# Kernel optimization log

Hardware: AMD Instinct MI355X
Metric: run time of the kernel (lower is better)

## Reference

```python
import jax, jax.numpy as jnp
import numpy as np

B, C, H, W = 32, 512, 32, 32  # in_dims = token_dim = 512, num_heads = 1
D = 512  # token_dim * num_heads
EPS = 1e-12  # torch F.normalize eps


def l2norm(x, axis):
    n = jnp.sqrt(jnp.sum(x * x, axis=axis, keepdims=True))
    return x / jnp.maximum(n, EPS)


def setup_inputs() -> dict:
    key = jax.random.key(0)
    ks = jax.random.split(key, 10)
    s = 1.0 / np.sqrt(D)
    return {
        "x_4d": jax.random.normal(ks[0], (B, C, H, W), dtype=jnp.float32),
        "Wq": jax.random.uniform(ks[1], (D, D), jnp.float32, -s, s),
        "bq": jax.random.uniform(ks[2], (D,), jnp.float32, -s, s),
        "Wk": jax.random.uniform(ks[3], (D, D), jnp.float32, -s, s),
        "bk": jax.random.uniform(ks[4], (D,), jnp.float32, -s, s),
        "w_g": jax.random.normal(ks[5], (D, 1), dtype=jnp.float32),
        "Wp": jax.random.uniform(ks[6], (D, D), jnp.float32, -s, s),
        "bp": jax.random.uniform(ks[7], (D,), jnp.float32, -s, s),
        "Wf": jax.random.uniform(ks[8], (D, D), jnp.float32, -s, s),
        "bf": jax.random.uniform(ks[9], (D,), jnp.float32, -s, s),
    }


def reference(x_4d, Wq, bq, Wk, bk, w_g, Wp, bp, Wf, bf):
    b, c, h, w = x_4d.shape
    n = h * w
    scale = D ** (-0.5)
    x = x_4d.reshape(b, c, n).transpose(0, 2, 1)  # [b, n, c]
    query = l2norm(jnp.einsum("bnc,dc->bnd", x, Wq) + bq, axis=-1)  # [b, n, d]
    key = l2norm(jnp.einsum("bnc,dc->bnd", x, Wk) + bk, axis=-1)    # [b, n, d]
    query_weight = query @ w_g                      # [b, n, 1]
    a = l2norm(query_weight * scale, axis=1)        # normalize over sequence dim
    g = jnp.sum(a * query, axis=1)                  # [b, d] global context
    out = jnp.einsum("bnd,ed->bne", g[:, None, :] * key, Wp) + bp + query
    out = jnp.einsum("bnd,ed->bne", out, Wf) + bf
    return out.transpose(0, 2, 1).reshape(b, c, h, w)
```

## Files before the change

### kernel.cpp

```cpp
#include <hip/hip_runtime.h>
#include <math.h>

#define B_ 32
#define D_ 512
#define N_ 1024
#define T_ 32768
#define SCALE 0.04419417382415922f

typedef unsigned short u16;
typedef __attribute__((ext_vector_type(8))) short bf16x8;
typedef __attribute__((ext_vector_type(4))) float f32x4;
typedef __attribute__((ext_vector_type(8))) unsigned short u16x8;

__device__ __forceinline__ u16 bf16_rn(float f) {
    unsigned u = __float_as_uint(f);
    u += 0x7FFFu + ((u >> 16) & 1u);
    return (u16)(u >> 16);
}
__device__ __forceinline__ float bf16f(u16 h) {
    return __uint_as_float(((unsigned)h) << 16);
}

__device__ __forceinline__ void g2l16(const u16* g, u16* lds) {
    __builtin_amdgcn_global_load_lds(
        (const __attribute__((address_space(1))) unsigned int*)g,
        (__attribute__((address_space(3))) unsigned int*)lds, 16, 0, 0);
}

__device__ __forceinline__ float waveRedSum(float v) {
#pragma unroll
    for (int off = 32; off > 0; off >>= 1) v += __shfl_xor(v, off, 64);
    return v;
}


__global__ __launch_bounds__(256) void convx_k(const float* __restrict__ x,
                                               u16* __restrict__ X) {
    __shared__ float tile[64][65];
    const int tid = threadIdx.x;
    const int n0 = blockIdx.x * 64, c0 = blockIdx.y * 64, b = blockIdx.z;
    const int nl = tid & 63, cl0 = (tid >> 6) * 16;
#pragma unroll
    for (int j = 0; j < 16; ++j)
        tile[cl0 + j][nl] = x[((size_t)(b * D_ + c0 + cl0 + j) << 10) + n0 + nl];
    __syncthreads();
    const int nr = tid >> 2, cb = (tid & 3) * 16;
    const size_t row = (size_t)(b * N_ + n0 + nr) * D_ + c0 + cb;
    u16 th[16];
#pragma unroll
    for (int j = 0; j < 16; ++j) th[j] = bf16_rn(tile[cb + j][nr]);
    *(u16x8*)&X[row]     = *(const u16x8*)&th[0];
    *(u16x8*)&X[row + 8] = *(const u16x8*)&th[8];
}

__global__ __launch_bounds__(256) void convw_k(const float* __restrict__ W0,
                                               const float* __restrict__ W1,
                                               const float* __restrict__ W2,
                                               u16* O0, u16* O1, u16* O2) {
    const int s = blockIdx.y;
    const float* src = (s == 0) ? W0 : ((s == 1) ? W1 : W2);
    u16* O = (s == 0) ? O0 : ((s == 1) ? O1 : O2);
    const size_t i0 = (size_t)blockIdx.x * 2048 + threadIdx.x * 8;
    u16 o[8];
#pragma unroll
    for (int j = 0; j < 8; ++j) o[j] = bf16_rn(src[i0 + j]);
    *(u16x8*)&O[i0] = *(const u16x8*)&o[0];
}


__global__ __launch_bounds__(256) void finalize_k(float* __restrict__ ssqQ,
                                                  float* __restrict__ ssqK,
                                                  float* __restrict__ qwr,
                                                  float* __restrict__ Sb) {
    __shared__ float red[4];
    const int i = blockIdx.x * 256 + threadIdx.x;
    const float rq = 1.f / fmaxf(sqrtf(ssqQ[i]), 1e-12f);
    ssqQ[i] = rq;
    const float rk = 1.f / fmaxf(sqrtf(ssqK[i]), 1e-12f);
    ssqK[i] = rk;
    const float qwp = qwr[i] * rq;
    qwr[i] = qwp * rq;
    float s = qwp * qwp;
    s = waveRedSum(s);
    if ((threadIdx.x & 63) == 0) red[threadIdx.x >> 6] = s;
    __syncthreads();
    if (threadIdx.x == 0)
        atomicAdd(Sb + (blockIdx.x >> 2), red[0] + red[1] + red[2] + red[3]);
}

__global__ __launch_bounds__(512) void gctx_k(const float* __restrict__ qw,
                                              const u16* __restrict__ Qn,
                                              float* __restrict__ g) {
    const int b = blockIdx.y;
    const int n0 = blockIdx.x * 128;
    const int d = threadIdx.x;
    const u16* qp = Qn + ((size_t)b * N_ + n0) * D_ + d;
    const float* wp = qw + (size_t)b * N_ + n0;
    float acc = 0.f;
    for (int n = 0; n < 128; ++n) acc += wp[n] * bf16f(qp[(size_t)n * D_]);
    atomicAdd(g + b * D_ + d, acc);
}

__global__ __launch_bounds__(256) void scalewp_k(const float* __restrict__ Wp,
                                                 const float* __restrict__ g,
                                                 const float* __restrict__ Sb,
                                                 u16* __restrict__ WpG) {
    const int b = blockIdx.y;
    const float fb = SCALE / fmaxf(SCALE * sqrtf(Sb[b]), 1e-12f);
    const size_t f0 = (size_t)blockIdx.x * 2048 + threadIdx.x * 8;
    const int c = (int)(f0 & 511);
    u16 o[8];
#pragma unroll
    for (int j = 0; j < 8; ++j)
        o[j] = bf16_rn(Wp[f0 + j] * g[b * D_ + c + j] * fb);
    *(u16x8*)&WpG[(size_t)b * 262144 + f0] = *(const u16x8*)&o[0];
}

__global__ __launch_bounds__(512) void mgemm0(
        const u16* __restrict__ A, const u16* __restrict__ B0,
        const u16* __restrict__ B1,
        const float* __restrict__ bias0, const float* __restrict__ bias1,
        const float* __restrict__ wg,
        float* __restrict__ ssqQ, float* __restrict__ ssqK,
        float* __restrict__ qwr, u16* uout0, u16* uout1) {
    __shared__ u16 As[128 * 64];
    __shared__ u16 Bs[256 * 64];
    const int tid = threadIdx.x;
    const int l = tid & 63, w = tid >> 6;
    const int gid = blockIdx.x;
    const int xcd = gid & 7;
    const int bx = (gid >> 3) & 3;
    const int by = (gid >> 5) * 8 + xcd;
    const int t0 = by * 128;
    const bool sel = bx >= 2;
    const int e0 = (bx & 1) * 256;
    const u16* B = sel ? B1 : B0;
    const float* bias = sel ? bias1 : bias0;
    u16* uout = sel ? uout1 : uout0;
    float* ssq = sel ? ssqK : ssqQ;

    size_t gA[2], gB[4];
    u16 *ldsA[2], *ldsB[4];
#pragma unroll
    for (int i = 0; i < 2; ++i) {
        const int rr = w * 16 + i * 8 + (l >> 3);
        gA[i] = (size_t)(t0 + rr) * 512 + (((l & 7) ^ (rr & 7)) * 8);
        ldsA[i] = As + (w * 16 + i * 8) * 64;
    }
#pragma unroll
    for (int i = 0; i < 4; ++i) {
        const int rr = w * 32 + i * 8 + (l >> 3);
        gB[i] = (size_t)(e0 + rr) * 512 + (((l & 7) ^ (rr & 7)) * 8);
        ldsB[i] = Bs + (w * 32 + i * 8) * 64;
    }

    const int wr = w >> 2, wc = w & 3, kg = l >> 4, r16 = l & 15;
    int aoff[4][2], boff[4][2];
#pragma unroll
    for (int f = 0; f < 4; ++f)
#pragma unroll
        for (int h = 0; h < 2; ++h) {
            const int ra = wr * 64 + f * 16 + r16;
            aoff[f][h] = ra * 64 + (((h * 4 + kg) ^ (ra & 7)) * 8);
            const int rb = wc * 64 + f * 16 + r16;
            boff[f][h] = rb * 64 + (((h * 4 + kg) ^ (rb & 7)) * 8);
        }

    f32x4 acc[4][4];
#pragma unroll
    for (int i = 0; i < 4; ++i)
#pragma unroll
        for (int j = 0; j < 4; ++j) acc[i][j] = 0.f;

#pragma unroll 1
    for (int c0 = 0; c0 < 512; c0 += 64) {
        __syncthreads();
#pragma unroll
        for (int i = 0; i < 2; ++i) g2l16(A + gA[i] + c0, ldsA[i]);
#pragma unroll
        for (int i = 0; i < 4; ++i) g2l16(B + gB[i] + c0, ldsB[i]);
        __syncthreads();
#pragma unroll
        for (int h = 0; h < 2; ++h) {
            bf16x8 av[4], bv[4];
#pragma unroll
            for (int f = 0; f < 4; ++f) {
                av[f] = *(const bf16x8*)&As[aoff[f][h]];
                bv[f] = *(const bf16x8*)&Bs[boff[f][h]];
            }
#pragma unroll
            for (int i = 0; i < 4; ++i)
#pragma unroll
                for (int j = 0; j < 4; ++j)
                    acc[i][j] = __builtin_amdgcn_mfma_f32_16x16x32_bf16(
                        av[i], bv[j], acc[i][j], 0, 0, 0);
        }
    }

    const int mb = wr * 64 + kg * 4;
    const int nb = wc * 64 + r16;
    float bb[4], wgv[4];
#pragma unroll
    for (int fn = 0; fn < 4; ++fn) {
        const int n = e0 + nb + fn * 16;
        bb[fn] = bias[n];
        wgv[fn] = sel ? 0.f : wg[n];
    }
#pragma unroll
    for (int fm = 0; fm < 4; ++fm) {
#pragma unroll
        for (int q = 0; q < 4; ++q) {
            const int m = t0 + mb + fm * 16 + q;
            float s2 = 0.f, wd = 0.f;
#pragma unroll
            for (int fn = 0; fn < 4; ++fn) {
                const float val = acc[fm][fn][q] + bb[fn];
                uout[(size_t)m * 512 + e0 + nb + fn * 16] = bf16_rn(val);
                s2 += val * val;
                wd += val * wgv[fn];
            }
#pragma unroll
            for (int off = 1; off < 16; off <<= 1) {
                s2 += __shfl_xor(s2, off, 64);
                wd += __shfl_xor(wd, off, 64);
            }
            if (r16 == 0) {
                atomicAdd(ssq + m, s2);
                if (!sel) atomicAdd(qwr + m, wd);
            }
        }
    }
}

template <int MODE>
__global__ __launch_bounds__(256) void mgemm12(
        const u16* __restrict__ A, const u16* __restrict__ B0,
        const float* __restrict__ bias,
        const float* __restrict__ rsA, const float* __restrict__ rsQ,
        u16* uout, float* __restrict__ fout) {
    __shared__ u16 As[128 * 64];
    __shared__ u16 Bs[128 * 64];
    const int tid = threadIdx.x;
    const int l = tid & 63, w = tid >> 6;
    const int gid = blockIdx.x;
    const int xcd = gid & 7;
    const int col = (gid >> 3) & 3;
    const int rowt = (gid >> 5) * 8 + xcd;

    const int t0 = rowt * 128 * (MODE == 1 ? 1 : 2) / (MODE == 1 ? 1 : 2);
    const int tt0 = rowt * 128;
    const int e0 = col * 128;
    const int batch = rowt >> 3;
    const u16* B = (MODE == 1) ? B0 + (size_t)batch * 262144 : B0;
    const int arow0 = (MODE == 2) ? e0 : tt0;
    const int brow0 = (MODE == 2) ? tt0 : e0;

    size_t gA[4], gB[4];
    u16 *ldsA[4], *ldsB[4];
#pragma unroll
    for (int i = 0; i < 4; ++i) {
        const int rr = w * 32 + i * 8 + (l >> 3);
        const int sw = ((l & 7) ^ (rr & 7)) * 8;
        gA[i] = (size_t)(arow0 + rr) * 512 + sw;
        gB[i] = (size_t)(brow0 + rr) * 512 + sw;
        ldsA[i] = As + (w * 32 + i * 8) * 64;
        ldsB[i] = Bs + (w * 32 + i * 8) * 64;
    }

    const int wr = w >> 1, wc = w & 1, kg = l >> 4, r16 = l & 15;
    int aoff[4][2], boff[4][2];
#pragma unroll
    for (int f = 0; f < 4; ++f)
#pragma unroll
        for (int h = 0; h < 2; ++h) {
            const int ra = wr * 64 + f * 16 + r16;
            aoff[f][h] = ra * 64 + (((h * 4 + kg) ^ (ra & 7)) * 8);
            const int rb = wc * 64 + f * 16 + r16;
            boff[f][h] = rb * 64 + (((h * 4 + kg) ^ (rb & 7)) * 8);
        }

    f32x4 acc[4][4];
#pragma unroll
    for (int i = 0; i < 4; ++i)
#pragma unroll
        for (int j = 0; j < 4; ++j) acc[i][j] = 0.f;

#pragma unroll 1
    for (int c0 = 0; c0 < 512; c0 += 64) {
        __syncthreads();
#pragma unroll
        for (int i = 0; i < 4; ++i) {
            g2l16(A + gA[i] + c0, ldsA[i]);
            g2l16(B + gB[i] + c0, ldsB[i]);
        }
        __syncthreads();
#pragma unroll
        for (int h = 0; h < 2; ++h) {
            bf16x8 av[4], bv[4];
#pragma unroll
            for (int f = 0; f < 4; ++f) {
                av[f] = *(const bf16x8*)&As[aoff[f][h]];
                bv[f] = *(const bf16x8*)&Bs[boff[f][h]];
            }
#pragma unroll
            for (int i = 0; i < 4; ++i)
#pragma unroll
                for (int j = 0; j < 4; ++j)
                    acc[i][j] = __builtin_amdgcn_mfma_f32_16x16x32_bf16(
                        av[i], bv[j], acc[i][j], 0, 0, 0);
        }
    }

    const int mb = wr * 64 + kg * 4;
    const int nb = wc * 64 + r16;
    if (MODE == 1) {
#pragma unroll
        for (int fm = 0; fm < 4; ++fm) {
            const int m0 = tt0 + mb + fm * 16;
            const float4 ra4 = *(const float4*)(rsA + m0);
            const float4 rq4 = *(const float4*)(rsQ + m0);
            const float ra_[4] = {ra4.x, ra4.y, ra4.z, ra4.w};
            const float rq_[4] = {rq4.x, rq4.y, rq4.z, rq4.w};
#pragma unroll
            for (int fn = 0; fn < 4; ++fn) {
                const int n = e0 + nb + fn * 16;
                const float bb = bias[n];
#pragma unroll
                for (int q = 0; q < 4; ++q) {
                    const size_t idx = (size_t)(m0 + q) * 512 + n;
                    const float val = acc[fm][fn][q] * ra_[q] + bb +
                                      bf16f(uout[idx]) * rq_[q];
                    uout[idx] = bf16_rn(val);
                }
            }
        }
    } else {
#pragma unroll
        for (int fm = 0; fm < 4; ++fm)
#pragma unroll
            for (int fn = 0; fn < 4; ++fn) {
                const int ntok = (tt0 & 1023) + nb + fn * 16;
#pragma unroll
                for (int q = 0; q < 4; ++q) {
                    const int e = e0 + mb + fm * 16 + q;
                    fout[((size_t)(batch * D_ + e) << 10) + ntok] =
                        acc[fm][fn][q] + bias[e];
                }
            }
    }
}


extern "C" void kernel_launch(void* const* d_in, const int* in_sizes, int n_in,
                              void* d_out, int out_size, void* d_ws, size_t ws_size,
                              hipStream_t stream) {
    const float* x  = (const float*)d_in[0];
    const float* Wq = (const float*)d_in[1];
    const float* bq = (const float*)d_in[2];
    const float* Wk = (const float*)d_in[3];
    const float* bk = (const float*)d_in[4];
    const float* wg = (const float*)d_in[5];
    const float* Wp = (const float*)d_in[6];
    const float* bp = (const float*)d_in[7];
    const float* Wf = (const float*)d_in[8];
    const float* bf = (const float*)d_in[9];
    float* out = (float*)d_out;

    char* Wb = (char*)d_ws;
    u16* Xbf = (u16*)Wb;
    u16* WpG = (u16*)Wb;
    u16* Qn  = (u16*)(Wb + 33554432ull);
    u16* Kn  = (u16*)(Wb + 67108864ull);
    char* S  = Wb + 100663296ull;
    u16* Wqbf = (u16*)S;
    u16* Wkbf = (u16*)(S + 524288ull);
    u16* Wfbf = (u16*)(S + 1048576ull);
    char* Z   = S + 1572864ull;
    float* SSQQ = (float*)Z;
    float* SSQK = (float*)(Z + 131072ull);
    float* QWR  = (float*)(Z + 262144ull);
    float* G    = (float*)(Z + 393216ull);
    float* Sb   = (float*)(Z + 458752ull);
    const size_t ZBYTES = 458752ull + 128ull;

    const dim3 blk(256);

    convx_k<<<dim3(16, 8, 32), blk, 0, stream>>>(x, Xbf);
    convw_k<<<dim3(128, 3), blk, 0, stream>>>(Wq, Wk, Wf, Wqbf, Wkbf, Wfbf);
    hipMemsetAsync(Z, 0, ZBYTES, stream);
    mgemm0<<<dim3(1024), dim3(512), 0, stream>>>(Xbf, Wqbf, Wkbf, bq, bk, wg,
                                                 SSQQ, SSQK, QWR, Qn, Kn);
    finalize_k<<<dim3(128), blk, 0, stream>>>(SSQQ, SSQK, QWR, Sb);
    gctx_k<<<dim3(8, B_), dim3(512), 0, stream>>>(QWR, Qn, G);
    scalewp_k<<<dim3(128, B_), blk, 0, stream>>>(Wp, G, Sb, WpG);
    mgemm12<1><<<dim3(1024), blk, 0, stream>>>(Kn, WpG, bp, SSQK, SSQQ, Qn,
                                               nullptr);
    mgemm12<2><<<dim3(1024), blk, 0, stream>>>(Wfbf, Qn, bf, nullptr, nullptr,
                                               nullptr, out);
}
```

Baseline: 157.1 us.

## Fuse x transpose and bf16 conversion into QK GEMM; remap MODE1 grid by batch

Removes the standalone convx_k kernel. The QK GEMM now reads fp32 x directly in its native [b,c,n] layout, converts it to bf16 in registers and writes it transposed into a padded LDS tile. The next K-slice of x is prefetched into registers while the current tile is consumed, and launch bounds request more waves. Separately, the MODE 1 GEMM block mapping groups the tiles of each batch on the same XCD, aiming at better cache reuse of the per-batch scaled Wp. In exchange, the conversion work is repeated across column blocks and x loads are strided, so global read traffic in the GEMM rises.

```diff
diff --git a/kernel.cpp b/kernel.cpp
--- a/kernel.cpp
+++ b/kernel.cpp
@@ -33,25 +33,6 @@
     return v;
 }
 
-
-__global__ __launch_bounds__(256) void convx_k(const float* __restrict__ x,
-                                               u16* __restrict__ X) {
-    __shared__ float tile[64][65];
-    const int tid = threadIdx.x;
-    const int n0 = blockIdx.x * 64, c0 = blockIdx.y * 64, b = blockIdx.z;
-    const int nl = tid & 63, cl0 = (tid >> 6) * 16;
-#pragma unroll
-    for (int j = 0; j < 16; ++j)
-        tile[cl0 + j][nl] = x[((size_t)(b * D_ + c0 + cl0 + j) << 10) + n0 + nl];
-    __syncthreads();
-    const int nr = tid >> 2, cb = (tid & 3) * 16;
-    const size_t row = (size_t)(b * N_ + n0 + nr) * D_ + c0 + cb;
-    u16 th[16];
-#pragma unroll
-    for (int j = 0; j < 16; ++j) th[j] = bf16_rn(tile[cb + j][nr]);
-    *(u16x8*)&X[row]     = *(const u16x8*)&th[0];
-    *(u16x8*)&X[row + 8] = *(const u16x8*)&th[8];
-}
 
 __global__ __launch_bounds__(256) void convw_k(const float* __restrict__ W0,
                                                const float* __restrict__ W1,
@@ -116,14 +97,14 @@
     *(u16x8*)&WpG[(size_t)b * 262144 + f0] = *(const u16x8*)&o[0];
 }
 
-__global__ __launch_bounds__(512) void mgemm0(
-        const u16* __restrict__ A, const u16* __restrict__ B0,
+__global__ __launch_bounds__(512, 4) void mgemm0(
+        const float* __restrict__ x, const u16* __restrict__ B0,
         const u16* __restrict__ B1,
         const float* __restrict__ bias0, const float* __restrict__ bias1,
         const float* __restrict__ wg,
         float* __restrict__ ssqQ, float* __restrict__ ssqK,
         float* __restrict__ qwr, u16* uout0, u16* uout1) {
-    __shared__ u16 As[128 * 64];
+    __shared__ u16 As[128 * 72];
     __shared__ u16 Bs[256 * 64];
     const int tid = threadIdx.x;
     const int l = tid & 63, w = tid >> 6;
@@ -139,14 +120,12 @@
     u16* uout = sel ? uout1 : uout0;
     float* ssq = sel ? ssqK : ssqQ;
 
-    size_t gA[2], gB[4];
-    u16 *ldsA[2], *ldsB[4];
-#pragma unroll
-    for (int i = 0; i < 2; ++i) {
-        const int rr = w * 16 + i * 8 + (l >> 3);
-        gA[i] = (size_t)(t0 + rr) * 512 + (((l & 7) ^ (rr & 7)) * 8);
-        ldsA[i] = As + (w * 16 + i * 8) * 64;
-    }
+    const int tr = tid & 127;
+    const int csl = (tid >> 7) * 16;
+    const float* xrow = x + (((size_t)((t0 >> 10) * D_ + csl)) << 10) +
+                        (t0 & 1023) + tr;
+    size_t gB[4];
+    u16* ldsB[4];
 #pragma unroll
     for (int i = 0; i < 4; ++i) {
         const int rr = w * 32 + i * 8 + (l >> 3);
@@ -161,7 +140,7 @@
 #pragma unroll
         for (int h = 0; h < 2; ++h) {
             const int ra = wr * 64 + f * 16 + r16;
-            aoff[f][h] = ra * 64 + (((h * 4 + kg) ^ (ra & 7)) * 8);
+            aoff[f][h] = ra * 72 + (h * 4 + kg) * 8;
             const int rb = wc * 64 + f * 16 + r16;
             boff[f][h] = rb * 64 + (((h * 4 + kg) ^ (rb & 7)) * 8);
         }
@@ -172,13 +151,26 @@
 #pragma unroll
         for (int j = 0; j < 4; ++j) acc[i][j] = 0.f;
 
+    float ar[16];
+#pragma unroll
+    for (int j = 0; j < 16; ++j) ar[j] = xrow[(size_t)j << 10];
+
 #pragma unroll 1
-    for (int c0 = 0; c0 < 512; c0 += 64) {
+    for (int s = 0; s < 8; ++s) {
+        const int c0 = s * 64;
         __syncthreads();
-#pragma unroll
-        for (int i = 0; i < 2; ++i) g2l16(A + gA[i] + c0, ldsA[i]);
+        u16 pk[16];
+#pragma unroll
+        for (int j = 0; j < 16; ++j) pk[j] = bf16_rn(ar[j]);
+        *(u16x8*)&As[tr * 72 + csl]     = *(const u16x8*)&pk[0];
+        *(u16x8*)&As[tr * 72 + csl + 8] = *(const u16x8*)&pk[8];
 #pragma unroll
         for (int i = 0; i < 4; ++i) g2l16(B + gB[i] + c0, ldsB[i]);
+        if (s < 7) {
+#pragma unroll
+            for (int j = 0; j < 16; ++j)
+                ar[j] = xrow[(size_t)(c0 + 64 + j) << 10];
+        }
         __syncthreads();
 #pragma unroll
         for (int h = 0; h < 2; ++h) {
@@ -244,13 +236,21 @@
     const int l = tid & 63, w = tid >> 6;
     const int gid = blockIdx.x;
     const int xcd = gid & 7;
-    const int col = (gid >> 3) & 3;
-    const int rowt = (gid >> 5) * 8 + xcd;
-
-    const int t0 = rowt * 128 * (MODE == 1 ? 1 : 2) / (MODE == 1 ? 1 : 2);
+
+    int rowt, col, batch;
+    if (MODE == 1) {
+        const int j = gid >> 3;
+        batch = (j >> 5) * 8 + xcd;
+        const int r = j & 31;
+        rowt = batch * 8 + (r >> 2);
+        col = r & 3;
+    } else {
+        col = (gid >> 3) & 3;
+        rowt = (gid >> 5) * 8 + xcd;
+        batch = rowt >> 3;
+    }
     const int tt0 = rowt * 128;
     const int e0 = col * 128;
-    const int batch = rowt >> 3;
     const u16* B = (MODE == 1) ? B0 + (size_t)batch * 262144 : B0;
     const int arow0 = (MODE == 2) ? e0 : tt0;
     const int brow0 = (MODE == 2) ? tt0 : e0;
@@ -367,7 +367,6 @@
     float* out = (float*)d_out;
 
     char* Wb = (char*)d_ws;
-    u16* Xbf = (u16*)Wb;
     u16* WpG = (u16*)Wb;
     u16* Qn  = (u16*)(Wb + 33554432ull);
     u16* Kn  = (u16*)(Wb + 67108864ull);
@@ -385,10 +384,9 @@
 
     const dim3 blk(256);
 
-    convx_k<<<dim3(16, 8, 32), blk, 0, stream>>>(x, Xbf);
     convw_k<<<dim3(128, 3), blk, 0, stream>>>(Wq, Wk, Wf, Wqbf, Wkbf, Wfbf);
     hipMemsetAsync(Z, 0, ZBYTES, stream);
-    mgemm0<<<dim3(1024), dim3(512), 0, stream>>>(Xbf, Wqbf, Wkbf, bq, bk, wg,
+    mgemm0<<<dim3(1024), dim3(512), 0, stream>>>(x, Wqbf, Wkbf, bq, bk, wg,
                                                  SSQQ, SSQK, QWR, Qn, Kn);
     finalize_k<<<dim3(128), blk, 0, stream>>>(SSQQ, SSQK, QWR, Sb);
     gctx_k<<<dim3(8, B_), dim3(512), 0, stream>>>(QWR, Qn, G);
```

Result: faster. 149.5 us (-4.9%).
